# Kernel optimization log

Hardware: AMD Instinct MI355X
Metric: run time of the kernel (lower is better)

## Reference

```python
import jax, jax.numpy as jnp
import numpy as np

K = 20          # neighbors (args.k)
NEG = 0.2       # LeakyReLU slope
EPS = 1e-8      # torch cosine_similarity eps


def knn_idx(x, k):
    # x: [B,C,N] -> idx [B,N,k] of nearest neighbors (largest -dist^2)
    xx = jnp.sum(x * x, axis=1)                       # [B,N]
    inner = jnp.einsum('bcn,bcm->bnm', x, x)          # [B,N,N]
    pd = 2.0 * inner - xx[:, :, None] - xx[:, None, :]
    return jax.lax.top_k(pd, k)[1]


def gather_neighbors(x, idx):
    # x: [B,C,N], idx: [B,N,K] -> [B,N,K,C]
    xt = jnp.transpose(x, (0, 2, 1))
    return jax.vmap(lambda f, i: f[i])(xt, idx)


def lrelu(x):
    return jnp.where(x >= 0, x, NEG * x)


def conv2d_bn(x, W, s, b):
    # 1x1 conv + inference BN (folded into scale s / bias b) + LeakyReLU; x: [B,C,N,K]
    y = jnp.einsum('oc,bcnk->bonk', W, x)
    return lrelu(y * s[None, :, None, None] + b[None, :, None, None])


def conv1d_bn(x, W, s, b):
    y = jnp.einsum('oc,bcn->bon', W, x)
    return lrelu(y * s[None, :, None] + b[None, :, None])


def manifold_weight(xyz, nor):
    # vectorized form of the original per-point double loop:
    # cosine similarity between nearest neighbor's normal (self) and all K neighbor normals
    idx = knn_idx(xyz, K)
    ng = gather_neighbors(nor, idx)                   # [B,N,K,3]
    c = ng[:, :, :1, :]                               # centroid normal [B,N,1,3]
    num = jnp.sum(c * ng, axis=-1)                    # [B,N,K]
    den = jnp.maximum(jnp.linalg.norm(c, axis=-1) * jnp.linalg.norm(ng, axis=-1), EPS)
    return num / den


def edge_stage(x, weight, w_mp, s_mp, b_mp):
    # get_graph_feature(concat=False) * conv_mp(weight), then concat center feats
    B, C, N = x.shape
    idx = knn_idx(x, K)
    neigh = gather_neighbors(x, idx)                  # [B,N,K,C]
    nf = jnp.transpose(neigh - jnp.transpose(x, (0, 2, 1))[:, :, None, :], (0, 3, 1, 2))  # [B,C,N,K]
    w = jnp.broadcast_to(weight[:, None, :, :], (B, C, N, K))
    nf = nf * conv2d_bn(w, w_mp, s_mp, b_mp)
    xc = jnp.broadcast_to(x[:, :, :, None], (B, C, N, K))
    return jnp.concatenate([nf, xc], axis=1)          # [B,2C,N,K]


def setup_inputs() -> dict:
    key = jax.random.key(0)
    keys = jax.random.split(key, 100)
    ki = iter(range(100))
    def nrm(shape, scale):
        return jax.random.normal(keys[next(ki)], shape, jnp.float32) * scale
    B, N = 8, 2048
    inp = {'xyznxnynz': nrm((B, 6, N), 1.0)}
    def add(name, cout, cin):
        inp['w' + name] = nrm((cout, cin), 1.0 / np.sqrt(cin))
        inp['s' + name] = 1.0 + nrm((cout,), 0.1)   # folded BN scale
        inp['b' + name] = nrm((cout,), 0.1)         # folded BN bias
    add('_mp1', 3, 3); add('_mp2', 64, 64); add('_mp3', 64, 64)
    add('1', 64, 6); add('2', 64, 64); add('3', 64, 128); add('4', 64, 64); add('5', 64, 128)
    add('6', 1024, 192); add('7', 256, 1216); add('8', 256, 256); add('9', 128, 256)
    inp['w10'] = nrm((50, 128), 1.0 / np.sqrt(128))
    return inp


def reference(xyznxnynz, w_mp1, s_mp1, b_mp1, w_mp2, s_mp2, b_mp2, w_mp3, s_mp3, b_mp3,
              w1, s1, b1, w2, s2, b2, w3, s3, b3, w4, s4, b4, w5, s5, b5,
              w6, s6, b6, w7, s7, b7, w8, s8, b8, w9, s9, b9, w10):
    xyz = xyznxnynz[:, :3, :]
    nor = xyznxnynz[:, 3:, :]
    N = xyz.shape[2]
    weight = manifold_weight(xyz, nor)                # [B,N,K]

    h = edge_stage(xyz, weight, w_mp1, s_mp1, b_mp1)  # [B,6,N,K]
    h = conv2d_bn(h, w1, s1, b1)
    h = conv2d_bn(h, w2, s2, b2)
    x1 = jnp.max(h, axis=-1)                          # [B,64,N]

    h = edge_stage(x1, weight, w_mp2, s_mp2, b_mp2)   # [B,128,N,K]
    h = conv2d_bn(h, w3, s3, b3)
    h = conv2d_bn(h, w4, s4, b4)
    x2 = jnp.max(h, axis=-1)

    h = edge_stage(x2, weight, w_mp3, s_mp3, b_mp3)
    h = conv2d_bn(h, w5, s5, b5)
    x3 = jnp.max(h, axis=-1)

    x = jnp.concatenate([x1, x2, x3], axis=1)         # [B,192,N]
    x = conv1d_bn(x, w6, s6, b6)                      # [B,1024,N]
    g = jnp.max(x, axis=-1, keepdims=True)
    g = jnp.broadcast_to(g, (g.shape[0], g.shape[1], N))
    x = jnp.concatenate([g, x1, x2, x3], axis=1)      # [B,1216,N]
    x = conv1d_bn(x, w7, s7, b7)
    x = conv1d_bn(x, w8, s8, b8)                      # dropout = identity (eval mode)
    x = conv1d_bn(x, w9, s9, b9)
    return jnp.einsum('oc,bcn->bon', w10, x)          # [B,50,N]
```

## Files before the change

### kernel.cpp

```cpp
#include <hip/hip_runtime.h>
#include <hip/hip_bf16.h>

#define NPT 2048
#define NB 8
#define KNN 20

__device__ __forceinline__ float bf2f(unsigned short u) {
    return __uint_as_float(((unsigned)u) << 16);
}
__device__ __forceinline__ unsigned short f2bf(float f) {
    unsigned u = __float_as_uint(f);
    unsigned lsb = (u >> 16) & 1u;
    u += 0x7fffu + lsb;
    return (unsigned short)(u >> 16);
}
__device__ __forceinline__ float lrelu(float x) { return x >= 0.f ? x : 0.2f * x; }
__device__ __forceinline__ float ldin(const void* p, size_t i, bool f32) {
    return f32 ? ((const float*)p)[i] : bf2f(((const unsigned short*)p)[i]);
}
__device__ __forceinline__ float rfl(float x) {
    return __int_as_float(__builtin_amdgcn_readfirstlane(__float_as_int(x)));
}
__device__ __forceinline__ unsigned long long mkkey64(float d, int m) {
    unsigned u = __float_as_uint(d);
    unsigned p = u ^ (unsigned)(((int)u >> 31) | 0x80000000);
    return ((unsigned long long)p << 11) | (unsigned)(2047 - m);
}
__device__ __forceinline__ unsigned long long shfl_xor_u64(unsigned long long v, int off) {
    unsigned lo = (unsigned)__shfl_xor((int)(unsigned)(v & 0xFFFFFFFFull), off);
    unsigned hi = (unsigned)__shfl_xor((int)(unsigned)(v >> 32), off);
    return ((unsigned long long)hi << 32) | lo;
}

template<int SH, int STR, int LM, int MK>
__device__ __forceinline__ void select_topk_d(const float* __restrict__ d, int lane, int* mymp) {
    unsigned long long b1 = 0ull, b2 = 0ull;
    #pragma unroll
    for (int s = 0; s < 32; s++) {
        int m = (s >> SH)*STR + lane*LM + (s & MK);
        unsigned long long v = mkkey64(d[s], m);
        bool gt1 = v > b1;
        unsigned long long nb2 = gt1 ? b1 : (v > b2 ? v : b2);
        b1 = gt1 ? v : b1;
        b2 = nb2;
    }
    unsigned long long lastpop = ~0ull;
    int mym = 0;
    #pragma unroll 1
    for (int k = 0; k < KNN; k++) {
        unsigned long long best = b1;
        #pragma unroll
        for (int off = 32; off > 0; off >>= 1) {
            unsigned long long o = shfl_xor_u64(best, off);
            best = o > best ? o : best;
        }
        if (lane == k) mym = 2047 - (int)(best & 2047ull);
        bool won = (b1 == best) && (best != 0ull);
        if (won) { lastpop = b1; b1 = b2; b2 = 0ull; }
        bool dirty = won && (b1 == 0ull);
        if (__ballot(dirty)) {
            if (dirty) {
                unsigned long long n1 = 0ull, n2 = 0ull;
                #pragma unroll
                for (int s = 0; s < 32; s++) {
                    int m = (s >> SH)*STR + lane*LM + (s & MK);
                    unsigned long long v = mkkey64(d[s], m);
                    v = (v < lastpop) ? v : 0ull;
                    bool gt1 = v > n1;
                    unsigned long long t2 = gt1 ? n1 : (v > n2 ? v : n2);
                    n1 = gt1 ? v : n1;
                    n2 = t2;
                }
                b1 = n1; b2 = n2;
            }
        }
    }
    *mymp = mym;
}

constexpr size_t F_IDX1  = 0;
constexpr size_t F_IDX2  = 327680;
constexpr size_t F_WT    = 655360;
constexpr size_t F_XCATT = 983040;
constexpr size_t F_XCAT  = 4128768;
constexpr size_t F_GPART = 7274496;
constexpr size_t F_G     = 7405568;
constexpr size_t F_V7P   = 7413760;
constexpr size_t F_V7    = 7430144;
constexpr size_t F_WP    = 7432192;
constexpr size_t F_FLAG  = 8074048;
constexpr size_t F_XX    = 8074052;
constexpr size_t F_X7    = 0;
constexpr size_t F_X8    = 2097152;
constexpr size_t F_X9    = 4194304;
constexpr size_t F_TOTAL = 8090436;

constexpr size_t P_AMP1 = 0;
constexpr size_t P_BMP1 = 64;
constexpr size_t P_AMP2 = 128;
constexpr size_t P_BMP2 = 192;
constexpr size_t P_AMP3 = 256;
constexpr size_t P_BMP3 = 320;
constexpr size_t P_W1   = 384;
constexpr size_t P_B1   = 896;
constexpr size_t P_W2   = 960;
constexpr size_t P_B2   = 5056;
constexpr size_t P_W3A  = 5120;
constexpr size_t P_W3B  = 9216;
constexpr size_t P_B3   = 13312;
constexpr size_t P_W4   = 13376;
constexpr size_t P_B4   = 17472;
constexpr size_t P_W5A  = 17536;
constexpr size_t P_W5B  = 21632;
constexpr size_t P_B5   = 25728;
constexpr size_t P_W6   = 25792;
constexpr size_t P_B6   = 222400;
constexpr size_t P_W7A  = 223424;
constexpr size_t P_W7B  = 485568;
constexpr size_t P_B7   = 534720;
constexpr size_t P_W8   = 534976;
constexpr size_t P_B8   = 600512;
constexpr size_t P_W9   = 600768;
constexpr size_t P_B9   = 633536;
constexpr size_t P_W10  = 633664;

struct InPtrs { const void* p[38]; };

__global__ __launch_bounds__(256) void zero_out_kernel(unsigned short* out, int nelem) {
    int i = blockIdx.x * 256 + threadIdx.x;
    if (i < nelem) out[i] = 0;
}

__global__ __launch_bounds__(256) void detect_kernel(const unsigned short* __restrict__ u,
                                                     int* __restrict__ flag) {
    __shared__ int red[256];
    int tid = threadIdx.x;
    int cnt = 0;
    for (int i = tid * 2; i < 98304; i += 512) {
        unsigned e = (u[i] >> 7) & 0xFFu;
        cnt += (e == 0xFFu) ? 1 : 0;
    }
    red[tid] = cnt;
    __syncthreads();
    for (int s = 128; s > 0; s >>= 1) {
        if (tid < s) red[tid] += red[tid + s];
        __syncthreads();
    }
    if (tid == 0) flag[0] = (red[0] > 8) ? 1 : 0;
}

__global__ __launch_bounds__(256) void prep_kernel(InPtrs in, float* __restrict__ wp,
                                                   const int* __restrict__ dflag) {
    bool f32 = dflag[0] != 0;
    int gtid = blockIdx.x * 256 + threadIdx.x;
    int gstr = gridDim.x * 256;
    if (gtid < 192) {
        int which = gtid >> 6, o = gtid & 63;
        const void *w, *s, *bb; int cin, cout; size_t ao, bo;
        if (which == 0)      { w = in.p[1]; s = in.p[2]; bb = in.p[3]; cin = 3;  cout = 3;  ao = P_AMP1; bo = P_BMP1; }
        else if (which == 1) { w = in.p[4]; s = in.p[5]; bb = in.p[6]; cin = 64; cout = 64; ao = P_AMP2; bo = P_BMP2; }
        else                 { w = in.p[7]; s = in.p[8]; bb = in.p[9]; cin = 64; cout = 64; ao = P_AMP3; bo = P_BMP3; }
        if (o < cout) {
            float sum = 0.f;
            for (int c = 0; c < cin; c++) sum += ldin(w, o*cin + c, f32);
            wp[ao + o] = sum * ldin(s, o, f32);
            wp[bo + o] = ldin(bb, o, f32);
        }
    }
    for (int i = gtid; i < 512; i += gstr) {
        int q = i & 3, o = (i >> 2) & 63, cc = i >> 8, c = cc*4 + q;
        wp[P_W1 + i] = (c < 6) ? ldin(in.p[10], o*6 + c, f32) * ldin(in.p[11], o, f32) : 0.f;
    }
    for (int i = gtid; i < 64; i += gstr) wp[P_B1 + i] = ldin(in.p[12], i, f32);
    for (int i = gtid; i < 4096; i += gstr) {
        int q = i & 3, o = (i >> 2) & 63, cc = i >> 8;
        wp[P_W2 + i] = ldin(in.p[13], o*64 + cc*4 + q, f32) * ldin(in.p[14], o, f32);
    }
    for (int i = gtid; i < 64; i += gstr) wp[P_B2 + i] = ldin(in.p[15], i, f32);
    for (int i = gtid; i < 4096; i += gstr) {
        int q = i & 3, o = (i >> 2) & 63, cc = i >> 8;
        float sc = ldin(in.p[17], o, f32);
        wp[P_W3A + i] = ldin(in.p[16], o*128 + cc*4 + q, f32) * sc;
        wp[P_W3B + i] = ldin(in.p[16], o*128 + 64 + cc*4 + q, f32) * sc;
    }
    for (int i = gtid; i < 64; i += gstr) wp[P_B3 + i] = ldin(in.p[18], i, f32);
    for (int i = gtid; i < 4096; i += gstr) {
        int q = i & 3, o = (i >> 2) & 63, cc = i >> 8;
        wp[P_W4 + i] = ldin(in.p[19], o*64 + cc*4 + q, f32) * ldin(in.p[20], o, f32);
    }
    for (int i = gtid; i < 64; i += gstr) wp[P_B4 + i] = ldin(in.p[21], i, f32);
    for (int i = gtid; i < 4096; i += gstr) {
        int q = i & 3, o = (i >> 2) & 63, cc = i >> 8;
        float sc = ldin(in.p[23], o, f32);
        wp[P_W5A + i] = ldin(in.p[22], o*128 + cc*4 + q, f32) * sc;
        wp[P_W5B + i] = ldin(in.p[22], o*128 + 64 + cc*4 + q, f32) * sc;
    }
    for (int i = gtid; i < 64; i += gstr) wp[P_B5 + i] = ldin(in.p[24], i, f32);
    for (int i = gtid; i < 192*1024; i += gstr) {
        int o = i & 1023, c = i >> 10;
        wp[P_W6 + i] = ldin(in.p[25], o*192 + c, f32) * ldin(in.p[26], o, f32);
    }
    for (int i = gtid; i < 1024; i += gstr) wp[P_B6 + i] = ldin(in.p[27], i, f32);
    for (int i = gtid; i < 1024*256; i += gstr) {
        int o = i & 255, c = i >> 8;
        wp[P_W7A + i] = ldin(in.p[28], o*1216 + c, f32) * ldin(in.p[29], o, f32);
    }
    for (int i = gtid; i < 192*256; i += gstr) {
        int o = i & 255, c = i >> 8;
        wp[P_W7B + i] = ldin(in.p[28], o*1216 + 1024 + c, f32) * ldin(in.p[29], o, f32);
    }
    for (int i = gtid; i < 256; i += gstr) wp[P_B7 + i] = ldin(in.p[30], i, f32);
    for (int i = gtid; i < 256*256; i += gstr) {
        int o = i & 255, c = i >> 8;
        wp[P_W8 + i] = ldin(in.p[31], o*256 + c, f32) * ldin(in.p[32], o, f32);
    }
    for (int i = gtid; i < 256; i += gstr) wp[P_B8 + i] = ldin(in.p[33], i, f32);
    for (int i = gtid; i < 256*128; i += gstr) {
        int o = i & 127, c = i >> 7;
        wp[P_W9 + i] = ldin(in.p[34], o*256 + c, f32) * ldin(in.p[35], o, f32);
    }
    for (int i = gtid; i < 128; i += gstr) wp[P_B9 + i] = ldin(in.p[36], i, f32);
    for (int i = gtid; i < 128*64; i += gstr) {
        int o = i & 63, c = i >> 6;
        wp[P_W10 + i] = (o < 50) ? ldin(in.p[37], o*128 + c, f32) : 0.f;
    }
}

__global__ __launch_bounds__(256) void knn_xyz_kernel(const void* __restrict__ xin,
                                                      const int* __restrict__ dflag,
                                                      int* __restrict__ idx_out,
                                                      float* __restrict__ wt_out) {
    bool f32 = dflag[0] != 0;
    int lane = threadIdx.x & 63, wid = threadIdx.x >> 6;
    int p = blockIdx.x * 4 + wid;
    int b = p >> 11, n = p & 2047;
    size_t eb = (size_t)b * 6 * NPT;
    float cx0 = ldin(xin, eb + n, f32), cx1 = ldin(xin, eb + NPT + n, f32), cx2 = ldin(xin, eb + 2*NPT + n, f32);
    float xxn = __builtin_fmaf(cx2, cx2, __builtin_fmaf(cx1, cx1, cx0*cx0));
    float d[32];
    #pragma unroll
    for (int j4 = 0; j4 < 8; j4++) {
        int m0 = j4*256 + lane*4;
        float x0q[4], x1q[4], x2q[4];
        if (f32) {
            const float* xf = (const float*)xin + eb;
            float4 a0 = *(const float4*)(xf + m0);
            float4 a1 = *(const float4*)(xf + NPT + m0);
            float4 a2 = *(const float4*)(xf + 2*NPT + m0);
            x0q[0]=a0.x; x0q[1]=a0.y; x0q[2]=a0.z; x0q[3]=a0.w;
            x1q[0]=a1.x; x1q[1]=a1.y; x1q[2]=a1.z; x1q[3]=a1.w;
            x2q[0]=a2.x; x2q[1]=a2.y; x2q[2]=a2.z; x2q[3]=a2.w;
        } else {
            const unsigned short* xu = (const unsigned short*)xin + eb;
            ushort4 a0 = *(const ushort4*)(xu + m0);
            ushort4 a1 = *(const ushort4*)(xu + NPT + m0);
            ushort4 a2 = *(const ushort4*)(xu + 2*NPT + m0);
            x0q[0]=bf2f(a0.x); x0q[1]=bf2f(a0.y); x0q[2]=bf2f(a0.z); x0q[3]=bf2f(a0.w);
            x1q[0]=bf2f(a1.x); x1q[1]=bf2f(a1.y); x1q[2]=bf2f(a1.z); x1q[3]=bf2f(a1.w);
            x2q[0]=bf2f(a2.x); x2q[1]=bf2f(a2.y); x2q[2]=bf2f(a2.z); x2q[3]=bf2f(a2.w);
        }
        #pragma unroll
        for (int q = 0; q < 4; q++) {
            float x0 = x0q[q], x1 = x1q[q], x2 = x2q[q];
            float inner = __builtin_fmaf(x2, cx2, __builtin_fmaf(x1, cx1, x0*cx0));
            float xxm   = __builtin_fmaf(x2, x2,  __builtin_fmaf(x1, x1,  x0*x0));
            d[j4*4 + q] = __builtin_fmaf(2.f, inner, -xxn) - xxm;
        }
    }
    int mym;
    select_topk_d<2,256,4,3>(d, lane, &mym);
    if (lane < KNN) idx_out[(size_t)p*KNN + lane] = mym;
    int m0n = __shfl(mym, 0);
    if (lane < KNN) {
        size_t nb0 = eb + 3*NPT;
        float c0 = ldin(xin, nb0 + m0n, f32), c1 = ldin(xin, nb0 + NPT + m0n, f32), c2 = ldin(xin, nb0 + 2*NPT + m0n, f32);
        float g0 = ldin(xin, nb0 + mym, f32), g1 = ldin(xin, nb0 + NPT + mym, f32), g2 = ldin(xin, nb0 + 2*NPT + mym, f32);
        float cn = sqrtf(__builtin_fmaf(c2, c2, __builtin_fmaf(c1, c1, c0*c0)));
        float gn = sqrtf(__builtin_fmaf(g2, g2, __builtin_fmaf(g1, g1, g0*g0)));
        float num = __builtin_fmaf(c2, g2, __builtin_fmaf(c1, g1, c0*g0));
        wt_out[(size_t)p*KNN + lane] = num / fmaxf(cn * gn, 1e-8f);
    }
}

__global__ __launch_bounds__(512) void norms_kernel(const float* __restrict__ xcat, int inRow,
                                                    float* __restrict__ xxg) {
    int t = blockIdx.x * 512 + threadIdx.x;
    int b = t >> 11, m = t & 2047;
    const float* xb = xcat + ((size_t)b*192 + inRow) * NPT + m;
    float s = 0.f;
    #pragma unroll
    for (int c = 0; c < 64; c++) { float v = xb[(size_t)c*NPT]; s = __builtin_fmaf(v, v, s); }
    xxg[t] = s;
}

__global__ __launch_bounds__(512) void knn_feat_kernel(const float* __restrict__ xcat,
        const float* __restrict__ xcatT, const float* __restrict__ xxg,
        int inOff, int* __restrict__ idx_out) {
    __shared__ float xmL[64][132];
    int tid = threadIdx.x, lane = tid & 63, wid = tid >> 6;
    int p = blockIdx.x * 8 + wid;
    int b = p >> 11, n = p & 2047;
    const float* xb = xcat + ((size_t)b*192 + inOff) * NPT;
    const float* qg = xcatT + ((size_t)(b*NPT + n))*192 + inOff;
    float q[64];
    #pragma unroll
    for (int c4 = 0; c4 < 16; c4++) {
        float4 v = *(const float4*)(qg + c4*4);
        q[c4*4+0] = rfl(v.x); q[c4*4+1] = rfl(v.y);
        q[c4*4+2] = rfl(v.z); q[c4*4+3] = rfl(v.w);
    }
    float xxn = xxg[b*2048 + n];
    float d[32];
    #pragma unroll
    for (int ch = 0; ch < 16; ch++) {
        __syncthreads();
        #pragma unroll
        for (int i = 0; i < 4; i++) {
            int idx4 = tid + i*512;
            int c = idx4 >> 5, m4 = (idx4 & 31) * 4;
            *(float4*)&xmL[c][m4] = *(const float4*)(xb + (size_t)c*NPT + ch*128 + m4);
        }
        __syncthreads();
        float in0 = 0.f, in1 = 0.f;
        #pragma unroll
        for (int c = 0; c < 64; c++) {
            float2 v = *(const float2*)&xmL[c][2*lane];
            in0 = __builtin_fmaf(q[c], v.x, in0);
            in1 = __builtin_fmaf(q[c], v.y, in1);
        }
        float2 xxv = *(const float2*)&xxg[b*2048 + ch*128 + 2*lane];
        d[ch*2]   = __builtin_fmaf(2.f, in0, -xxn) - xxv.x;
        d[ch*2+1] = __builtin_fmaf(2.f, in1, -xxn) - xxv.y;
    }
    int mym;
    select_topk_d<1,128,2,1>(d, lane, &mym);
    if (lane < KNN) idx_out[(size_t)p*KNN + lane] = mym;
}

__global__ __launch_bounds__(64) void stage1_kernel(const void* __restrict__ xin,
        const int* __restrict__ dflag,
        const int* __restrict__ idxb, const float* __restrict__ wtb,
        const float* __restrict__ wp, float* __restrict__ xcat, float* __restrict__ xcatT) {
    __shared__ float y1L[KNN][64];
    bool f32 = dflag[0] != 0;
    int lane = threadIdx.x & 63;
    int p = blockIdx.x, b = p >> 11, n = p & 2047;
    size_t eb = (size_t)b * 6 * NPT;
    int myidx = 0; float mywt = 0.f;
    if (lane < KNN) {
        myidx = idxb[(size_t)p*KNN + lane] & 2047;
        mywt  = wtb[(size_t)p*KNN + lane];
    }
    float cx0 = ldin(xin, eb + n, f32), cx1 = ldin(xin, eb + NPT + n, f32), cx2 = ldin(xin, eb + 2*NPT + n, f32);
    float aM0 = wp[P_AMP1+0], aM1 = wp[P_AMP1+1], aM2 = wp[P_AMP1+2];
    float bM0 = wp[P_BMP1+0], bM1 = wp[P_BMP1+1], bM2 = wp[P_BMP1+2];
    float w1r[8];
    #pragma unroll
    for (int cc = 0; cc < 2; cc++) {
        float4 v = *(const float4*)&wp[P_W1 + (size_t)(cc*64 + lane)*4];
        w1r[cc*4+0] = v.x; w1r[cc*4+1] = v.y; w1r[cc*4+2] = v.z; w1r[cc*4+3] = v.w;
    }
    float b1v = wp[P_B1 + lane];
    #pragma unroll
    for (int k = 0; k < KNN; k++) {
        int m = __shfl(myidx, k);
        float w = __shfl(mywt, k);
        float n0 = ldin(xin, eb + m, f32), n1 = ldin(xin, eb + NPT + m, f32), n2 = ldin(xin, eb + 2*NPT + m, f32);
        float h0 = (n0 - cx0) * lrelu(fmaf(aM0, w, bM0));
        float h1 = (n1 - cx1) * lrelu(fmaf(aM1, w, bM1));
        float h2 = (n2 - cx2) * lrelu(fmaf(aM2, w, bM2));
        float acc = w1r[0]*h0 + w1r[1]*h1 + w1r[2]*h2 + w1r[3]*cx0 + w1r[4]*cx1 + w1r[5]*cx2;
        y1L[k][lane] = lrelu(acc + b1v);
    }
    float acc2[KNN];
    #pragma unroll
    for (int k = 0; k < KNN; k++) acc2[k] = 0.f;
    #pragma unroll
    for (int cc = 0; cc < 16; cc++) {
        float4 w4 = *(const float4*)&wp[P_W2 + (size_t)(cc*64 + lane)*4];
        #pragma unroll
        for (int k = 0; k < KNN; k++) {
            float4 h4 = *(const float4*)&y1L[k][cc*4];
            float a = acc2[k];
            a = fmaf(w4.x, h4.x, a); a = fmaf(w4.y, h4.y, a);
            a = fmaf(w4.z, h4.z, a); a = fmaf(w4.w, h4.w, a);
            acc2[k] = a;
        }
    }
    float b2v = wp[P_B2 + lane];
    float mx = -1e38f;
    #pragma unroll
    for (int k = 0; k < KNN; k++) mx = fmaxf(mx, lrelu(acc2[k] + b2v));
    xcat[((size_t)b*192 + lane)*NPT + n] = mx;
    xcatT[((size_t)(b*NPT + n))*192 + lane] = mx;
}

__global__ __launch_bounds__(64) void stage23_kernel(
        const float* __restrict__ xcatT, const int* __restrict__ idxb, const float* __restrict__ wtb,
        const float* __restrict__ wp,
        int aOff, int bmpOff, int WaOff, int WbOff, int biasOff,
        int W2Off, int bias2Off, int inOff, int outCh, int second,
        float* __restrict__ xcat, float* __restrict__ xcatTo) {
    __shared__ float hL[KNN][64];
    __shared__ float cL[64];
    int lane = threadIdx.x & 63;
    int p = blockIdx.x, b = p >> 11, n = p & 2047;
    const float* xTb = xcatT + (size_t)b * NPT * 192 + inOff;
    int myidx = 0; float mywt = 0.f;
    if (lane < KNN) {
        myidx = idxb[(size_t)p*KNN + lane] & 2047;
        mywt  = wtb[(size_t)p*KNN + lane];
    }
    float cv = xTb[(size_t)n * 192 + lane];
    cL[lane] = cv;
    float aMP = wp[aOff + lane], bMP = wp[bmpOff + lane];
    #pragma unroll
    for (int k = 0; k < KNN; k++) {
        int m = __shfl(myidx, k);
        float w = __shfl(mywt, k);
        float nb = xTb[(size_t)m * 192 + lane];
        hL[k][lane] = (nb - cv) * lrelu(fmaf(aMP, w, bMP));
    }
    float vb = 0.f;
    #pragma unroll
    for (int cc = 0; cc < 16; cc++) {
        float4 w4 = *(const float4*)&wp[WbOff + (size_t)(cc*64 + lane)*4];
        float4 c4 = *(const float4*)&cL[cc*4];
        vb = fmaf(w4.x, c4.x, vb); vb = fmaf(w4.y, c4.y, vb);
        vb = fmaf(w4.z, c4.z, vb); vb = fmaf(w4.w, c4.w, vb);
    }
    float acc[KNN];
    #pragma unroll
    for (int k = 0; k < KNN; k++) acc[k] = 0.f;
    #pragma unroll
    for (int cc = 0; cc < 16; cc++) {
        float4 w4 = *(const float4*)&wp[WaOff + (size_t)(cc*64 + lane)*4];
        #pragma unroll
        for (int k = 0; k < KNN; k++) {
            float4 h4 = *(const float4*)&hL[k][cc*4];
            float a = acc[k];
            a = fmaf(w4.x, h4.x, a); a = fmaf(w4.y, h4.y, a);
            a = fmaf(w4.z, h4.z, a); a = fmaf(w4.w, h4.w, a);
            acc[k] = a;
        }
    }
    float bv = wp[biasOff + lane];
    float mx = -1e38f;
    if (second) {
        #pragma unroll
        for (int k = 0; k < KNN; k++) hL[k][lane] = lrelu(acc[k] + vb + bv);
        float acc2[KNN];
        #pragma unroll
        for (int k = 0; k < KNN; k++) acc2[k] = 0.f;
        #pragma unroll
        for (int cc = 0; cc < 16; cc++) {
            float4 w4 = *(const float4*)&wp[W2Off + (size_t)(cc*64 + lane)*4];
            #pragma unroll
            for (int k = 0; k < KNN; k++) {
                float4 h4 = *(const float4*)&hL[k][cc*4];
                float a = acc2[k];
                a = fmaf(w4.x, h4.x, a); a = fmaf(w4.y, h4.y, a);
                a = fmaf(w4.z, h4.z, a); a = fmaf(w4.w, h4.w, a);
                acc2[k] = a;
            }
        }
        float b2v = wp[bias2Off + lane];
        #pragma unroll
        for (int k = 0; k < KNN; k++) mx = fmaxf(mx, lrelu(acc2[k] + b2v));
    } else {
        #pragma unroll
        for (int k = 0; k < KNN; k++) mx = fmaxf(mx, lrelu(acc[k] + vb + bv));
    }
    xcat[((size_t)b*192 + outCh + lane)*NPT + n] = mx;
    xcatTo[((size_t)(b*NPT + n))*192 + outCh + lane] = mx;
}

template<int OUT, bool INBF, bool VBIAS>
__global__ __launch_bounds__(256) void gemm_kernel(
        const void* __restrict__ Xv, const float* __restrict__ WT,
        const float* __restrict__ bias, const float* __restrict__ vbias,
        unsigned short* __restrict__ Ybf, float* __restrict__ Yf,
        const int* __restrict__ dflag,
        int Cin, int strideW, int CoutY) {
    __shared__ float wL[16][68];
    __shared__ float xL[16][132];
    __shared__ float gred[64][17];
    int tid = threadIdx.x;
    int tx = tid & 15, ty = tid >> 4;
    int nt = blockIdx.x * 128, ot = blockIdx.y * 64, b = blockIdx.z;
    const float* Xf = (const float*)Xv;
    const unsigned short* Xs = (const unsigned short*)Xv;
    float acc[4][8];
    #pragma unroll
    for (int i = 0; i < 4; i++)
        #pragma unroll
        for (int j = 0; j < 8; j++) acc[i][j] = 0.f;
    for (int c0 = 0; c0 < Cin; c0 += 16) {
        __syncthreads();
        #pragma unroll
        for (int i = 0; i < 4; i++) {
            int idx = tid + i*256; int r = idx >> 6, o = idx & 63;
            wL[r][o] = WT[(size_t)(c0 + r) * strideW + ot + o];
        }
        #pragma unroll
        for (int i = 0; i < 8; i++) {
            int idx = tid + i*256; int r = idx >> 7, m = idx & 127;
            if (INBF) xL[r][m] = bf2f(Xs[(size_t)b * Cin * NPT + (size_t)(c0 + r) * NPT + nt + m]);
            else      xL[r][m] = Xf[(size_t)b * Cin * NPT + (size_t)(c0 + r) * NPT + nt + m];
        }
        __syncthreads();
        #pragma unroll
        for (int kk = 0; kk < 16; kk++) {
            float4 w4 = *(const float4*)&wL[kk][ty*4];
            float4 xa = *(const float4*)&xL[kk][tx*8];
            float4 xb4 = *(const float4*)&xL[kk][tx*8 + 4];
            float wv[4] = {w4.x, w4.y, w4.z, w4.w};
            float xv[8] = {xa.x, xa.y, xa.z, xa.w, xb4.x, xb4.y, xb4.z, xb4.w};
            #pragma unroll
            for (int oi = 0; oi < 4; oi++)
                #pragma unroll
                for (int j = 0; j < 8; j++)
                    acc[oi][j] = fmaf(wv[oi], xv[j], acc[oi][j]);
        }
    }
    if (OUT == 1) {
        #pragma unroll
        for (int oi = 0; oi < 4; oi++) {
            float bb = bias[ot + ty*4 + oi];
            float m = -1e38f;
            #pragma unroll
            for (int j = 0; j < 8; j++) m = fmaxf(m, lrelu(acc[oi][j] + bb));
            gred[ty*4 + oi][tx] = m;
        }
        __syncthreads();
        if (tid < 64) {
            float m = gred[tid][0];
            #pragma unroll
            for (int t = 1; t < 16; t++) m = fmaxf(m, gred[tid][t]);
            Yf[((size_t)b*16 + blockIdx.x)*1024 + ot + tid] = m;
        }
    } else if (OUT == 2) {
        bool f32 = dflag[0] != 0;
        #pragma unroll
        for (int oi = 0; oi < 4; oi++) {
            int o = ot + ty*4 + oi;
            if (o < 50) {
                size_t base = ((size_t)b*50 + o)*NPT + nt + tx*8;
                #pragma unroll
                for (int j = 0; j < 8; j++) {
                    if (f32) Yf[base + j] = acc[oi][j];
                    else     Ybf[base + j] = f2bf(acc[oi][j]);
                }
            }
        }
    } else {
        #pragma unroll
        for (int oi = 0; oi < 4; oi++) {
            int o = ot + ty*4 + oi;
            float bb = bias[o];
            if (VBIAS) bb += vbias[(size_t)b*256 + o];
            size_t base = ((size_t)b*CoutY + o)*NPT + nt + tx*8;
            #pragma unroll
            for (int j = 0; j < 8; j++) Ybf[base + j] = f2bf(lrelu(acc[oi][j] + bb));
        }
    }
}

__global__ __launch_bounds__(256) void gmax_reduce_kernel(const float* __restrict__ gpart, float* __restrict__ g) {
    int o = blockIdx.x * 256 + threadIdx.x;
    int b = blockIdx.y;
    float m = -1e38f;
    for (int ch = 0; ch < 16; ch++) m = fmaxf(m, gpart[((size_t)b*16 + ch)*1024 + o]);
    g[(size_t)b*1024 + o] = m;
}

__global__ __launch_bounds__(256) void v7_part_kernel(const float* __restrict__ wp, const float* __restrict__ g,
                                                      float* __restrict__ v7p) {
    int o = threadIdx.x, ch = blockIdx.x, b = blockIdx.y;
    __shared__ float gL[128];
    if (threadIdx.x < 128) gL[threadIdx.x] = g[(size_t)b*1024 + ch*128 + threadIdx.x];
    __syncthreads();
    float acc = 0.f;
    #pragma unroll 4
    for (int c = 0; c < 128; c++) acc = fmaf(wp[P_W7A + (size_t)(ch*128 + c)*256 + o], gL[c], acc);
    v7p[((size_t)b*8 + ch)*256 + o] = acc;
}

__global__ __launch_bounds__(256) void v7_sum_kernel(const float* __restrict__ v7p, float* __restrict__ v7) {
    int o = threadIdx.x, b = blockIdx.x;
    float acc = 0.f;
    #pragma unroll
    for (int ch = 0; ch < 8; ch++) acc += v7p[((size_t)b*8 + ch)*256 + o];
    v7[(size_t)b*256 + o] = acc;
}

extern "C" void kernel_launch(void* const* d_in, const int* in_sizes, int n_in,
                              void* d_out, int out_size, void* d_ws, size_t ws_size,
                              hipStream_t stream) {
    (void)in_sizes;
    if (n_in < 38 || ws_size < F_TOTAL * sizeof(float)) {
        int nb = (out_size + 255) / 256;
        hipLaunchKernelGGL(zero_out_kernel, dim3(nb), dim3(256), 0, stream,
                           (unsigned short*)d_out, out_size);
        return;
    }
    float* W = (float*)d_ws;
    InPtrs ptrs;
    for (int i = 0; i < 38; i++) ptrs.p[i] = d_in[i];
    int* idx1 = (int*)(W + F_IDX1);
    int* idx2 = (int*)(W + F_IDX2);
    float* wt = W + F_WT;
    float* xcat = W + F_XCAT;
    float* xcatT = W + F_XCATT;
    unsigned short* x7 = (unsigned short*)(W + F_X7);
    unsigned short* x8 = (unsigned short*)(W + F_X8);
    unsigned short* x9 = (unsigned short*)(W + F_X9);
    float* gpart = W + F_GPART;
    float* g = W + F_G;
    float* v7p = W + F_V7P;
    float* v7 = W + F_V7;
    float* wp = W + F_WP;
    int* dflag = (int*)(W + F_FLAG);
    float* xxg = W + F_XX;

    hipLaunchKernelGGL(detect_kernel, dim3(1), dim3(256), 0, stream,
                       (const unsigned short*)d_in[0], dflag);
    hipLaunchKernelGGL(prep_kernel, dim3(256), dim3(256), 0, stream, ptrs, wp, dflag);
    hipLaunchKernelGGL(knn_xyz_kernel, dim3(4096), dim3(256), 0, stream, d_in[0], dflag, idx1, wt);
    hipLaunchKernelGGL(stage1_kernel, dim3(16384), dim3(64), 0, stream, d_in[0], dflag, idx1, wt, wp, xcat, xcatT);
    hipLaunchKernelGGL(norms_kernel, dim3(32), dim3(512), 0, stream, xcat, 0, xxg);
    hipLaunchKernelGGL(knn_feat_kernel, dim3(2048), dim3(512), 0, stream, xcat, xcatT, xxg, 0, idx2);
    hipLaunchKernelGGL(stage23_kernel, dim3(16384), dim3(64), 0, stream, xcatT, idx2, wt, wp,
        (int)P_AMP2, (int)P_BMP2, (int)P_W3A, (int)P_W3B, (int)P_B3, (int)P_W4, (int)P_B4,
        0, 64, 1, xcat, xcatT);
    hipLaunchKernelGGL(norms_kernel, dim3(32), dim3(512), 0, stream, xcat, 64, xxg);
    hipLaunchKernelGGL(knn_feat_kernel, dim3(2048), dim3(512), 0, stream, xcat, xcatT, xxg, 64, idx2);
    hipLaunchKernelGGL(stage23_kernel, dim3(16384), dim3(64), 0, stream, xcatT, idx2, wt, wp,
        (int)P_AMP3, (int)P_BMP3, (int)P_W5A, (int)P_W5B, (int)P_B5, 0, 0,
        64, 128, 0, xcat, xcatT);
    hipLaunchKernelGGL((gemm_kernel<1,false,false>), dim3(16,16,8), dim3(256), 0, stream,
        (const void*)xcat, wp + P_W6, wp + P_B6, (const float*)nullptr,
        (unsigned short*)nullptr, gpart, dflag, 192, 1024, 1024);
    hipLaunchKernelGGL(gmax_reduce_kernel, dim3(4,8), dim3(256), 0, stream, gpart, g);
    hipLaunchKernelGGL(v7_part_kernel, dim3(8,8), dim3(256), 0, stream, wp, g, v7p);
    hipLaunchKernelGGL(v7_sum_kernel, dim3(8), dim3(256), 0, stream, v7p, v7);
    hipLaunchKernelGGL((gemm_kernel<0,false,true>), dim3(16,4,8), dim3(256), 0, stream,
        (const void*)xcat, wp + P_W7B, wp + P_B7, v7, x7, (float*)nullptr, dflag, 192, 256, 256);
    hipLaunchKernelGGL((gemm_kernel<0,true,false>), dim3(16,4,8), dim3(256), 0, stream,
        (const void*)x7, wp + P_W8, wp + P_B8, (const float*)nullptr, x8, (float*)nullptr, dflag, 256, 256, 256);
    hipLaunchKernelGGL((gemm_kernel<0,true,false>), dim3(16,2,8), dim3(256), 0, stream,
        (const void*)x8, wp + P_W9, wp + P_B9, (const float*)nullptr, x9, (float*)nullptr, dflag, 256, 128, 128);
    hipLaunchKernelGGL((gemm_kernel<2,true,false>), dim3(16,1,8), dim3(256), 0, stream,
        (const void*)x9, wp + P_W10, (const float*)nullptr, (const float*)nullptr,
        (unsigned short*)d_out, (float*)d_out, dflag, 128, 64, 50);
}
```

Before: 1.576 ms.

## Process two points per block and chunk neighbors by four in stage23 kernel

The edge-conv stage kernel now handles two points per 64-thread block, so each weight float4 loaded from global memory is reused for both points. Neighbors are processed in chunks of four with a running max instead of materializing all 20 hidden rows, which shrinks shared memory and the per-thread accumulator arrays. This cuts register pressure and weight-load traffic, at the cost of halving the grid size and serializing the neighbor loop (unroll 1). The chunked loop also has no barrier between shared writes and reads, which relies on the block being a single wavefront.

```diff
diff --git a/kernel.cpp b/kernel.cpp
--- a/kernel.cpp
+++ b/kernel.cpp
@@ -401,78 +401,113 @@
         int aOff, int bmpOff, int WaOff, int WbOff, int biasOff,
         int W2Off, int bias2Off, int inOff, int outCh, int second,
         float* __restrict__ xcat, float* __restrict__ xcatTo) {
-    __shared__ float hL[KNN][64];
-    __shared__ float cL[64];
+    __shared__ float hL[2][4][64];
+    __shared__ float cL[2][64];
     int lane = threadIdx.x & 63;
-    int p = blockIdx.x, b = p >> 11, n = p & 2047;
+    int p0 = blockIdx.x * 2, p1 = p0 + 1;
+    int b = p0 >> 11, n0 = p0 & 2047, n1 = n0 + 1;
     const float* xTb = xcatT + (size_t)b * NPT * 192 + inOff;
-    int myidx = 0; float mywt = 0.f;
+    int id0 = 0, id1 = 0; float wt0 = 0.f, wt1 = 0.f;
     if (lane < KNN) {
-        myidx = idxb[(size_t)p*KNN + lane] & 2047;
-        mywt  = wtb[(size_t)p*KNN + lane];
-    }
-    float cv = xTb[(size_t)n * 192 + lane];
-    cL[lane] = cv;
+        id0 = idxb[(size_t)p0*KNN + lane] & 2047;
+        wt0 = wtb[(size_t)p0*KNN + lane];
+        id1 = idxb[(size_t)p1*KNN + lane] & 2047;
+        wt1 = wtb[(size_t)p1*KNN + lane];
+    }
+    float cv0 = xTb[(size_t)n0 * 192 + lane];
+    float cv1 = xTb[(size_t)n1 * 192 + lane];
+    cL[0][lane] = cv0;
+    cL[1][lane] = cv1;
     float aMP = wp[aOff + lane], bMP = wp[bmpOff + lane];
-    #pragma unroll
-    for (int k = 0; k < KNN; k++) {
-        int m = __shfl(myidx, k);
-        float w = __shfl(mywt, k);
-        float nb = xTb[(size_t)m * 192 + lane];
-        hL[k][lane] = (nb - cv) * lrelu(fmaf(aMP, w, bMP));
-    }
-    float vb = 0.f;
+    float bv = wp[biasOff + lane];
+    float b2v = second ? wp[bias2Off + lane] : 0.f;
+    float vb0 = 0.f, vb1 = 0.f;
     #pragma unroll
     for (int cc = 0; cc < 16; cc++) {
         float4 w4 = *(const float4*)&wp[WbOff + (size_t)(cc*64 + lane)*4];
-        float4 c4 = *(const float4*)&cL[cc*4];
-        vb = fmaf(w4.x, c4.x, vb); vb = fmaf(w4.y, c4.y, vb);
-        vb = fmaf(w4.z, c4.z, vb); vb = fmaf(w4.w, c4.w, vb);
-    }
-    float acc[KNN];
-    #pragma unroll
-    for (int k = 0; k < KNN; k++) acc[k] = 0.f;
-    #pragma unroll
-    for (int cc = 0; cc < 16; cc++) {
-        float4 w4 = *(const float4*)&wp[WaOff + (size_t)(cc*64 + lane)*4];
-        #pragma unroll
-        for (int k = 0; k < KNN; k++) {
-            float4 h4 = *(const float4*)&hL[k][cc*4];
-            float a = acc[k];
-            a = fmaf(w4.x, h4.x, a); a = fmaf(w4.y, h4.y, a);
-            a = fmaf(w4.z, h4.z, a); a = fmaf(w4.w, h4.w, a);
-            acc[k] = a;
-        }
-    }
-    float bv = wp[biasOff + lane];
-    float mx = -1e38f;
-    if (second) {
-        #pragma unroll
-        for (int k = 0; k < KNN; k++) hL[k][lane] = lrelu(acc[k] + vb + bv);
-        float acc2[KNN];
-        #pragma unroll
-        for (int k = 0; k < KNN; k++) acc2[k] = 0.f;
+        float4 c40 = *(const float4*)&cL[0][cc*4];
+        float4 c41 = *(const float4*)&cL[1][cc*4];
+        vb0 = fmaf(w4.x, c40.x, vb0); vb0 = fmaf(w4.y, c40.y, vb0);
+        vb0 = fmaf(w4.z, c40.z, vb0); vb0 = fmaf(w4.w, c40.w, vb0);
+        vb1 = fmaf(w4.x, c41.x, vb1); vb1 = fmaf(w4.y, c41.y, vb1);
+        vb1 = fmaf(w4.z, c41.z, vb1); vb1 = fmaf(w4.w, c41.w, vb1);
+    }
+    float mx0 = -1e38f, mx1 = -1e38f;
+    #pragma unroll 1
+    for (int kc = 0; kc < KNN; kc += 4) {
+        #pragma unroll
+        for (int j = 0; j < 4; j++) {
+            int k = kc + j;
+            int m0 = __shfl(id0, k); float w0 = __shfl(wt0, k);
+            int m1 = __shfl(id1, k); float w1 = __shfl(wt1, k);
+            float nb0 = xTb[(size_t)m0 * 192 + lane];
+            float nb1 = xTb[(size_t)m1 * 192 + lane];
+            hL[0][j][lane] = (nb0 - cv0) * lrelu(fmaf(aMP, w0, bMP));
+            hL[1][j][lane] = (nb1 - cv1) * lrelu(fmaf(aMP, w1, bMP));
+        }
+        float a0[4], a1[4];
+        #pragma unroll
+        for (int j = 0; j < 4; j++) { a0[j] = 0.f; a1[j] = 0.f; }
         #pragma unroll
         for (int cc = 0; cc < 16; cc++) {
-            float4 w4 = *(const float4*)&wp[W2Off + (size_t)(cc*64 + lane)*4];
-            #pragma unroll
-            for (int k = 0; k < KNN; k++) {
-                float4 h4 = *(const float4*)&hL[k][cc*4];
-                float a = acc2[k];
-                a = fmaf(w4.x, h4.x, a); a = fmaf(w4.y, h4.y, a);
-                a = fmaf(w4.z, h4.z, a); a = fmaf(w4.w, h4.w, a);
-                acc2[k] = a;
+            float4 w4 = *(const float4*)&wp[WaOff + (size_t)(cc*64 + lane)*4];
+            #pragma unroll
+            for (int j = 0; j < 4; j++) {
+                float4 h0 = *(const float4*)&hL[0][j][cc*4];
+                float4 h1 = *(const float4*)&hL[1][j][cc*4];
+                float x = a0[j];
+                x = fmaf(w4.x, h0.x, x); x = fmaf(w4.y, h0.y, x);
+                x = fmaf(w4.z, h0.z, x); x = fmaf(w4.w, h0.w, x);
+                a0[j] = x;
+                float y = a1[j];
+                y = fmaf(w4.x, h1.x, y); y = fmaf(w4.y, h1.y, y);
+                y = fmaf(w4.z, h1.z, y); y = fmaf(w4.w, h1.w, y);
+                a1[j] = y;
             }
         }
-        float b2v = wp[bias2Off + lane];
-        #pragma unroll
-        for (int k = 0; k < KNN; k++) mx = fmaxf(mx, lrelu(acc2[k] + b2v));
-    } else {
-        #pragma unroll
-        for (int k = 0; k < KNN; k++) mx = fmaxf(mx, lrelu(acc[k] + vb + bv));
-    }
-    xcat[((size_t)b*192 + outCh + lane)*NPT + n] = mx;
-    xcatTo[((size_t)(b*NPT + n))*192 + outCh + lane] = mx;
+        if (second) {
+            #pragma unroll
+            for (int j = 0; j < 4; j++) {
+                hL[0][j][lane] = lrelu(a0[j] + vb0 + bv);
+                hL[1][j][lane] = lrelu(a1[j] + vb1 + bv);
+            }
+            float s0[4], s1[4];
+            #pragma unroll
+            for (int j = 0; j < 4; j++) { s0[j] = 0.f; s1[j] = 0.f; }
+            #pragma unroll
+            for (int cc = 0; cc < 16; cc++) {
+                float4 w4 = *(const float4*)&wp[W2Off + (size_t)(cc*64 + lane)*4];
+                #pragma unroll
+                for (int j = 0; j < 4; j++) {
+                    float4 h0 = *(const float4*)&hL[0][j][cc*4];
+                    float4 h1 = *(const float4*)&hL[1][j][cc*4];
+                    float x = s0[j];
+                    x = fmaf(w4.x, h0.x, x); x = fmaf(w4.y, h0.y, x);
+                    x = fmaf(w4.z, h0.z, x); x = fmaf(w4.w, h0.w, x);
+                    s0[j] = x;
+                    float y = s1[j];
+                    y = fmaf(w4.x, h1.x, y); y = fmaf(w4.y, h1.y, y);
+                    y = fmaf(w4.z, h1.z, y); y = fmaf(w4.w, h1.w, y);
+                    s1[j] = y;
+                }
+            }
+            #pragma unroll
+            for (int j = 0; j < 4; j++) {
+                mx0 = fmaxf(mx0, lrelu(s0[j] + b2v));
+                mx1 = fmaxf(mx1, lrelu(s1[j] + b2v));
+            }
+        } else {
+            #pragma unroll
+            for (int j = 0; j < 4; j++) {
+                mx0 = fmaxf(mx0, lrelu(a0[j] + vb0 + bv));
+                mx1 = fmaxf(mx1, lrelu(a1[j] + vb1 + bv));
+            }
+        }
+    }
+    xcat[((size_t)b*192 + outCh + lane)*NPT + n0] = mx0;
+    xcat[((size_t)b*192 + outCh + lane)*NPT + n1] = mx1;
+    xcatTo[((size_t)(b*NPT + n0))*192 + outCh + lane] = mx0;
+    xcatTo[((size_t)(b*NPT + n1))*192 + outCh + lane] = mx1;
 }
 
 template<int OUT, bool INBF, bool VBIAS>
@@ -630,12 +665,12 @@
     hipLaunchKernelGGL(stage1_kernel, dim3(16384), dim3(64), 0, stream, d_in[0], dflag, idx1, wt, wp, xcat, xcatT);
     hipLaunchKernelGGL(norms_kernel, dim3(32), dim3(512), 0, stream, xcat, 0, xxg);
     hipLaunchKernelGGL(knn_feat_kernel, dim3(2048), dim3(512), 0, stream, xcat, xcatT, xxg, 0, idx2);
-    hipLaunchKernelGGL(stage23_kernel, dim3(16384), dim3(64), 0, stream, xcatT, idx2, wt, wp,
+    hipLaunchKernelGGL(stage23_kernel, dim3(8192), dim3(64), 0, stream, xcatT, idx2, wt, wp,
         (int)P_AMP2, (int)P_BMP2, (int)P_W3A, (int)P_W3B, (int)P_B3, (int)P_W4, (int)P_B4,
         0, 64, 1, xcat, xcatT);
     hipLaunchKernelGGL(norms_kernel, dim3(32), dim3(512), 0, stream, xcat, 64, xxg);
     hipLaunchKernelGGL(knn_feat_kernel, dim3(2048), dim3(512), 0, stream, xcat, xcatT, xxg, 64, idx2);
-    hipLaunchKernelGGL(stage23_kernel, dim3(16384), dim3(64), 0, stream, xcatT, idx2, wt, wp,
+    hipLaunchKernelGGL(stage23_kernel, dim3(8192), dim3(64), 0, stream, xcatT, idx2, wt, wp,
         (int)P_AMP3, (int)P_BMP3, (int)P_W5A, (int)P_W5B, (int)P_B5, 0, 0,
         64, 128, 0, xcat, xcatT);
     hipLaunchKernelGGL((gemm_kernel<1,false,false>), dim3(16,16,8), dim3(256), 0, stream,
```

After: 1.588 ms. About the same (+0.8%).
